# Performance work log

Measured on AMD Instinct MI355X. Metric: run time of the kernel, lower is better.

## Reference

```python
import jax, jax.numpy as jnp
import numpy as np

S = 4096      # total packed tokens
DIM = 1280    # hidden dim
H = 16        # num heads
HD = DIM // H # head dim = 80


def setup_inputs() -> dict:
    key = jax.random.key(0)
    ks = jax.random.split(key, 5)
    hidden_states = jax.random.normal(ks[0], (S, DIM), jnp.float32)
    # realistic rotary tables: [S, HD] with duplicated half-frequencies
    inv_freq = 1.0 / (10000.0 ** (np.arange(0, HD // 2, dtype=np.float64) / (HD // 2)))
    ang = np.arange(S, dtype=np.float64)[:, None] * inv_freq[None, :]          # [S, HD/2]
    emb = np.concatenate([ang, ang], axis=-1)                                   # [S, HD]
    cos = jnp.asarray(np.cos(emb), jnp.float32)
    sin = jnp.asarray(np.sin(emb), jnp.float32)
    scale = 1.0 / np.sqrt(DIM)
    qkv_w = jax.random.normal(ks[1], (3 * DIM, DIM), jnp.float32) * scale
    qkv_b = jax.random.normal(ks[2], (3 * DIM,), jnp.float32) * 0.02
    proj_w = jax.random.normal(ks[3], (DIM, DIM), jnp.float32) * scale
    proj_b = jax.random.normal(ks[4], (DIM,), jnp.float32) * 0.02
    # ragged segment boundaries: must start at 0 and end at S
    cu_seqlens = jnp.asarray([0, 300, 900, 1500, 2300, 2900, 3500, 4000, 4096], jnp.int32)
    return {
        "hidden_states": hidden_states,
        "cos": cos,
        "sin": sin,
        "qkv_w": qkv_w,
        "qkv_b": qkv_b,
        "proj_w": proj_w,
        "proj_b": proj_b,
        "cu_seqlens": cu_seqlens,
    }


def _rotate_half(x):
    x1, x2 = jnp.split(x, 2, axis=-1)
    return jnp.concatenate([-x2, x1], axis=-1)


def reference(hidden_states, cos, sin, qkv_w, qkv_b, proj_w, proj_b, cu_seqlens):
    seq_len, dim = hidden_states.shape
    hd = dim // H
    qkv = (hidden_states @ qkv_w.T + qkv_b).reshape(seq_len, 3, H, hd)
    q, k, v = qkv[:, 0], qkv[:, 1], qkv[:, 2]                 # each [S, H, hd]
    # RoPE in float32, broadcast cos/sin over heads
    c = cos[:, None, :].astype(jnp.float32)
    s = sin[:, None, :].astype(jnp.float32)
    qf = q.astype(jnp.float32)
    kf = k.astype(jnp.float32)
    q = (qf * c + _rotate_half(qf) * s).astype(q.dtype)
    k = (kf * c + _rotate_half(kf) * s).astype(k.dtype)
    # block-diagonal additive mask: segment id per token
    pos = jnp.arange(seq_len)
    seg = jnp.searchsorted(cu_seqlens[1:], pos, side='right')  # [S]
    neg = jnp.finfo(jnp.float32).min
    bias = jnp.where(seg[:, None] == seg[None, :], 0.0, neg)   # [S, S]
    attn = jnp.einsum('shd,thd->hst', q, k) / np.sqrt(hd) + bias[None]
    w = jax.nn.softmax(attn.astype(jnp.float32), axis=-1).astype(q.dtype)
    out = jnp.einsum('hst,thd->shd', w, v).reshape(seq_len, dim)
    return out @ proj_w.T + proj_b
```

## Files before the change

kernel.cpp:

```cpp
#include <hip/hip_runtime.h>
#include <hip/hip_bf16.h>
#include <stdint.h>

#define SQ 4096
#define DM 1280
#define NH 16
#define HDIM 80
#define N_QKV 3840

typedef __attribute__((ext_vector_type(8))) short short8;
typedef __attribute__((ext_vector_type(4))) float f32x4;

__device__ __forceinline__ unsigned short f2bf(float f) {
  union { float f; unsigned int u; } v; v.f = f;
  unsigned int r = v.u + 0x7FFFu + ((v.u >> 16) & 1u);
  return (unsigned short)(r >> 16);
}
__device__ __forceinline__ float bf2f(unsigned short u) {
  union { unsigned int u; float f; } v; v.u = ((unsigned int)u) << 16;
  return v.f;
}

__global__ __launch_bounds__(256) void cvt_all(const float* __restrict__ hidden,
                                               const float* __restrict__ qkv_w,
                                               const float* __restrict__ proj_w,
                                               unsigned short* __restrict__ oh,
                                               unsigned short* __restrict__ oq,
                                               unsigned short* __restrict__ op) {
  int b = blockIdx.x;
  const float* in;
  unsigned short* out;
  int base;
  if (b < 5120) { in = hidden; out = oh; base = b; }
  else if (b < 9920) { in = qkv_w; out = oq; base = b - 5120; }
  else { in = proj_w; out = op; base = b - 9920; }
  int i = base * 256 + threadIdx.x;
  float4 v = reinterpret_cast<const float4*>(in)[i];
  ushort4 o;
  o.x = f2bf(v.x); o.y = f2bf(v.y); o.z = f2bf(v.z); o.w = f2bf(v.w);
  reinterpret_cast<ushort4*>(out)[i] = o;
}

__device__ __forceinline__ void gload_lds16(const void* g, void* l) {
  __builtin_amdgcn_global_load_lds(
      (const __attribute__((address_space(1))) void*)g,
      (__attribute__((address_space(3))) void*)l, 16, 0, 0);
}

template <int OUT_BF16>
__global__ __launch_bounds__(512, 4) void gemm_bt2(const unsigned short* __restrict__ A,
                                                   const unsigned short* __restrict__ B,
                                                   const float* __restrict__ bias,
                                                   void* __restrict__ C, int M, int N, int K,
                                                   int nbx) {
  __shared__ __align__(16) unsigned short As[3][256 * 32];
  __shared__ __align__(16) unsigned short Bs[3][128 * 32];
  const int tid = threadIdx.x;
  const int wave = tid >> 6, lane = tid & 63;
  const int r15 = lane & 15, kg = lane >> 4;
  const int wr = wave >> 1, wc = wave & 1;

  const int b = blockIdx.x;
  const int c = b & 7, i = b >> 3;
  const int by = (c & 3) * 4 + (i & 3);
  const int bx = (c >> 2) * (nbx >> 1) + (i >> 2);
  const int tm = by * 256, tn = bx * 128;

  f32x4 acc[4][4];
#pragma unroll
  for (int x = 0; x < 4; ++x)
#pragma unroll
    for (int j = 0; j < 4; ++j) acc[x][j] = {0.f, 0.f, 0.f, 0.f};

  const int rowt = tid >> 2, k8t = (tid & 3) << 3;
  const unsigned short* Arow0 = A + (size_t)(tm + rowt) * K + k8t;
  const unsigned short* Arow1 = Arow0 + (size_t)128 * K;
  const unsigned short* Brow = B + (size_t)(tn + rowt) * K + k8t;
  const int ldsA0 = tid * 8, ldsA1 = (512 + tid) * 8, ldsB = tid * 8;

  auto stage = [&](int kt, int buf) {
    gload_lds16(Arow0 + kt, &As[buf][ldsA0]);
    gload_lds16(Arow1 + kt, &As[buf][ldsA1]);
    gload_lds16(Brow + kt, &Bs[buf][ldsB]);
  };

  const int nk = K >> 5;
  stage(0, 0);
  stage(32, 1);

  int buf = 0;
  for (int t = 0; t < nk; ++t) {
    if (t + 2 < nk) {
      stage((t + 2) << 5, (buf + 2) % 3);
      asm volatile("s_waitcnt vmcnt(6)" ::: "memory");
    } else if (t + 1 < nk) {
      asm volatile("s_waitcnt vmcnt(3)" ::: "memory");
    } else {
      asm volatile("s_waitcnt vmcnt(0)" ::: "memory");
    }
    __builtin_amdgcn_sched_barrier(0);
    __builtin_amdgcn_s_barrier();

    short8 af[4], bfr[4];
#pragma unroll
    for (int mi = 0; mi < 4; ++mi)
      af[mi] = *reinterpret_cast<const short8*>(&As[buf][(wr * 64 + mi * 16 + r15) * 32 + kg * 8]);
#pragma unroll
    for (int ni = 0; ni < 4; ++ni)
      bfr[ni] = *reinterpret_cast<const short8*>(&Bs[buf][(wc * 64 + ni * 16 + r15) * 32 + kg * 8]);
    __builtin_amdgcn_s_setprio(1);
#pragma unroll
    for (int mi = 0; mi < 4; ++mi)
#pragma unroll
      for (int ni = 0; ni < 4; ++ni)
        acc[mi][ni] = __builtin_amdgcn_mfma_f32_16x16x32_bf16(af[mi], bfr[ni], acc[mi][ni], 0, 0, 0);
    __builtin_amdgcn_s_setprio(0);

    __builtin_amdgcn_s_barrier();
    __builtin_amdgcn_sched_barrier(0);
    buf = (buf + 1) % 3;
  }

#pragma unroll
  for (int mi = 0; mi < 4; ++mi) {
#pragma unroll
    for (int ni = 0; ni < 4; ++ni) {
      int col = tn + wc * 64 + ni * 16 + r15;
      float bv = bias[col];
#pragma unroll
      for (int r = 0; r < 4; ++r) {
        int row = tm + wr * 64 + mi * 16 + kg * 4 + r;
        float v = acc[mi][ni][r] + bv;
        if (OUT_BF16)
          ((unsigned short*)C)[(size_t)row * N + col] = f2bf(v);
        else
          ((float*)C)[(size_t)row * N + col] = v;
      }
    }
  }
}

__global__ __launch_bounds__(256) void rope_v_kernel(unsigned short* __restrict__ qkv,
                                                     const float* __restrict__ cosb,
                                                     const float* __restrict__ sinb,
                                                     unsigned short* __restrict__ Vt) {
  const float SC = 0.1118033988749895f;
  int h = blockIdx.y, s0 = blockIdx.x * 64;
  __shared__ unsigned short vt[64][80];
  for (int e = threadIdx.x; e < 64 * 40; e += 256) {
    int sl = e / 40, dp = e % 40;
    int s = s0 + sl;
    float c = cosb[s * HDIM + dp];
    float sn = sinb[s * HDIM + dp];
    size_t qb = (size_t)s * N_QKV + h * HDIM;
    float q1 = bf2f(qkv[qb + dp]), q2 = bf2f(qkv[qb + dp + 40]);
    qkv[qb + dp] = f2bf((q1 * c - q2 * sn) * SC);
    qkv[qb + dp + 40] = f2bf((q2 * c + q1 * sn) * SC);
    size_t kb = qb + DM;
    float k1 = bf2f(qkv[kb + dp]), k2 = bf2f(qkv[kb + dp + 40]);
    qkv[kb + dp] = f2bf(k1 * c - k2 * sn);
    qkv[kb + dp + 40] = f2bf(k2 * c + k1 * sn);
    size_t vb = qb + 2 * DM;
    vt[sl][dp] = qkv[vb + dp];
    vt[sl][dp + 40] = qkv[vb + dp + 40];
  }
  __syncthreads();
  for (int e = threadIdx.x; e < HDIM * 64; e += 256) {
    int d = e >> 6, sl = e & 63;
    Vt[((size_t)h * HDIM + d) * SQ + s0 + sl] = vt[sl][d];
  }
}

template <int CTRL>
__device__ __forceinline__ float dpp_f(float x) {
  int xi = __builtin_bit_cast(int, x);
  int r = __builtin_amdgcn_update_dpp(xi, xi, CTRL, 0xf, 0xf, true);
  return __builtin_bit_cast(float, r);
}
__device__ __forceinline__ float rowmax16(float x) {
  x = fmaxf(x, dpp_f<0xB1>(x));
  x = fmaxf(x, dpp_f<0x4E>(x));
  x = fmaxf(x, dpp_f<0x141>(x));
  x = fmaxf(x, dpp_f<0x140>(x));
  return x;
}
__device__ __forceinline__ float rowsum16(float x) {
  x += dpp_f<0xB1>(x);
  x += dpp_f<0x4E>(x);
  x += dpp_f<0x141>(x);
  x += dpp_f<0x140>(x);
  return x;
}

__global__ __launch_bounds__(256, 2) void attn_kernel(const unsigned short* __restrict__ qkv,
                                                      const unsigned short* __restrict__ Vt,
                                                      const int* __restrict__ cu, int nseg,
                                                      unsigned short* __restrict__ attn_out) {
  constexpr int PROW = 68;
  __shared__ __align__(16) unsigned char Kl[2][64 * 256];
  __shared__ __align__(16) unsigned char Vl[2][80 * 128];
  __shared__ __align__(16) unsigned short Pl[4][16 * PROW];
  __shared__ int cus[32];
  __shared__ int keyv[64];
  __shared__ unsigned char tile_of_rank[64];

  const int tid = threadIdx.x;
  const int wave = tid >> 6, lane = tid & 63;
  const int r15 = lane & 15, kg = lane >> 4;
  const int s7 = r15 & 7;
  const short8 z8 = {0, 0, 0, 0, 0, 0, 0, 0};

  const int b = blockIdx.x;
  const int xcd = b & 7, j = b >> 3;
  const int h = xcd * 2 + (j >> 6);

  if (tid <= nseg) cus[tid] = cu[tid];
  __syncthreads();

  auto seg_of = [&](int pos) {
    int s2 = 0;
    for (int i2 = 1; i2 < nseg; ++i2)
      if (pos >= cus[i2]) s2 = i2;
    return s2;
  };

  if (tid < 64) {
    int tb = tid * 64;
    int kb = cus[seg_of(tb)] & ~63;
    int ke = cus[seg_of(tb + 63) + 1];
    keyv[tid] = (ke - kb + 63) >> 6;
  }
  __syncthreads();
  if (tid < 64) {
    int mykey = keyv[tid];
    int rank = 0;
    for (int u = 0; u < 64; ++u) {
      int ku = keyv[u];
      rank += (ku > mykey) || (ku == mykey && u < tid);
    }
    tile_of_rank[rank] = (unsigned char)tid;
  }
  __syncthreads();
  const int qt = tile_of_rank[j & 63];

  const int tbase = qt * 64;
  const int wbase = tbase + wave * 16;
  int rs[4], re[4];
#pragma unroll
  for (int r = 0; r < 4; ++r) {
    int sg = seg_of(wbase + kg * 4 + r);
    rs[r] = cus[sg];
    re[r] = cus[sg + 1];
  }
  const int seg_lo = seg_of(wbase), seg_hi = seg_of(wbase + 15);
  const int w_lo = cus[seg_lo], w_hi = cus[seg_hi + 1];
  const int rs_hi = cus[seg_hi], re_lo = cus[seg_lo + 1];

  const int kb0 = cus[seg_of(tbase)] & ~63;
  const int kend = cus[seg_of(tbase + 63) + 1];
  const int nt = (kend - kb0 + 63) >> 6;

  const unsigned short* qp = qkv + (size_t)(wbase + r15) * N_QKV + h * HDIM;
  short8 qf[3];
#pragma unroll
  for (int ds = 0; ds < 3; ++ds) {
    int d0 = ds * 32 + kg * 8;
    qf[ds] = (d0 < HDIM) ? *reinterpret_cast<const short8*>(qp + d0) : z8;
  }

  float m[4] = {-1e30f, -1e30f, -1e30f, -1e30f};
  float l[4] = {0.f, 0.f, 0.f, 0.f};
  f32x4 acc[5];
#pragma unroll
  for (int dg = 0; dg < 5; ++dg) acc[dg] = {0.f, 0.f, 0.f, 0.f};

  const unsigned short* kbase = qkv + DM + (size_t)h * HDIM;
  const unsigned short* vbase = Vt + (size_t)h * HDIM * SQ;
  unsigned short* pw = &Pl[wave][0];
  const int wub = tid & ~63;

  auto issue_stage = [&](int kb, int buf) {
    unsigned char* kd = &Kl[buf][0];
    unsigned char* vd = &Vl[buf][0];
#pragma unroll
    for (int p = 0; p < 4; ++p) {
      int L = p * 256 + tid;
      int row = L >> 4;
      int c = (L & 15) ^ (row & 7);
      int csrc = (c < 10) ? c : 0;
      gload_lds16(kbase + (size_t)(kb + row) * N_QKV + csrc * 8,
                  kd + (p * 256 + wub) * 16);
    }
#pragma unroll
    for (int p = 0; p < 2; ++p) {
      int L = p * 256 + tid;
      int row = L >> 3;
      int c = (L & 7) ^ (row & 7);
      gload_lds16(vbase + (size_t)row * SQ + kb + c * 8,
                  vd + (p * 256 + wub) * 16);
    }
    {
      int L = 512 + (wub >> 1) + (lane & 31);
      int row = L >> 3;
      int c = (L & 7) ^ (row & 7);
      if (lane < 32)
        gload_lds16(vbase + (size_t)row * SQ + kb + c * 8,
                    vd + (512 + (wub >> 1)) * 16);
    }
  };

  issue_stage(kb0, 0);
  int cur = 0;

  for (int t = 0; t < nt; ++t) {
    const int k0 = kb0 + (t << 6);
    if (t + 1 < nt) {
      issue_stage(k0 + 64, cur ^ 1);
      asm volatile("s_waitcnt vmcnt(7)" ::: "memory");
    } else {
      asm volatile("s_waitcnt vmcnt(0)" ::: "memory");
    }
    __builtin_amdgcn_sched_barrier(0);
    __builtin_amdgcn_s_barrier();

    const bool active = (k0 < w_hi) && (k0 + 64 > w_lo);
    if (active) {
      const unsigned char* Kc = &Kl[cur][0];
      const unsigned char* Vc = &Vl[cur][0];

      f32x4 sa[4];
#pragma unroll
      for (int g = 0; g < 4; ++g) sa[g] = {0.f, 0.f, 0.f, 0.f};
#pragma unroll
      for (int g = 0; g < 4; ++g) {
        const unsigned char* kr = Kc + ((g * 16 + r15) << 8);
#pragma unroll
        for (int ds = 0; ds < 3; ++ds) {
          int d0 = ds * 32 + kg * 8;
          short8 kf = (d0 < HDIM)
              ? *reinterpret_cast<const short8*>(kr + (((ds * 4 + kg) ^ s7) << 4))
              : z8;
          sa[g] = __builtin_amdgcn_mfma_f32_16x16x32_bf16(qf[ds], kf, sa[g], 0, 0, 0);
        }
      }

      short8 vf[5][2];
#pragma unroll
      for (int dg = 0; dg < 5; ++dg)
#pragma unroll
        for (int g2 = 0; g2 < 2; ++g2)
          vf[dg][g2] = *reinterpret_cast<const short8*>(
              Vc + ((dg * 16 + r15) << 7) + (((g2 * 4 + kg) ^ s7) << 4));

      const bool interior = (k0 >= rs_hi) && (k0 + 64 <= re_lo);
      float corr[4];
      bool resc;
      if (interior) {
        float mx4[4];
#pragma unroll
        for (int r = 0; r < 4; ++r)
          mx4[r] = rowmax16(fmaxf(fmaxf(sa[0][r], sa[1][r]), fmaxf(sa[2][r], sa[3][r])));
        int defer = (mx4[0] <= m[0] + 8.f) && (mx4[1] <= m[1] + 8.f) &&
                    (mx4[2] <= m[2] + 8.f) && (mx4[3] <= m[3] + 8.f);
        if (__all(defer)) {
          resc = false;
#pragma unroll
          for (int r = 0; r < 4; ++r) {
            unsigned short* prow = pw + (kg * 4 + r) * PROW;
            float sm = 0.f;
#pragma unroll
            for (int g = 0; g < 4; ++g) {
              float pv = __expf(sa[g][r] - m[r]);
              sm += pv;
              prow[g * 16 + r15] = f2bf(pv);
            }
            l[r] += rowsum16(sm);
          }
        } else {
          resc = true;
#pragma unroll
          for (int r = 0; r < 4; ++r) {
            unsigned short* prow = pw + (kg * 4 + r) * PROW;
            float mn = fmaxf(m[r], mx4[r]);
            corr[r] = __expf(m[r] - mn);
            float sm = 0.f;
#pragma unroll
            for (int g = 0; g < 4; ++g) {
              float pv = __expf(sa[g][r] - mn);
              sm += pv;
              prow[g * 16 + r15] = f2bf(pv);
            }
            l[r] = l[r] * corr[r] + rowsum16(sm);
            m[r] = mn;
          }
        }
      } else {
        resc = true;
#pragma unroll
        for (int r = 0; r < 4; ++r) {
          unsigned short* prow = pw + (kg * 4 + r) * PROW;
          float vv[4];
#pragma unroll
          for (int g = 0; g < 4; ++g) {
            int key = k0 + g * 16 + r15;
            vv[g] = (key >= rs[r] && key < re[r]) ? sa[g][r] : -1e30f;
          }
          float mx = rowmax16(fmaxf(fmaxf(vv[0], vv[1]), fmaxf(vv[2], vv[3])));
          float mn = fmaxf(m[r], mx);
          corr[r] = __expf(m[r] - mn);
          float sm = 0.f;
#pragma unroll
          for (int g = 0; g < 4; ++g) {
            float pv = __expf(vv[g] - mn);
            sm += pv;
            prow[g * 16 + r15] = f2bf(pv);
          }
          l[r] = l[r] * corr[r] + rowsum16(sm);
          m[r] = mn;
        }
      }
      if (resc) {
#pragma unroll
        for (int dg = 0; dg < 5; ++dg) {
          f32x4 t2 = acc[dg];
          t2[0] *= corr[0]; t2[1] *= corr[1]; t2[2] *= corr[2]; t2[3] *= corr[3];
          acc[dg] = t2;
        }
      }

      asm volatile("s_waitcnt lgkmcnt(0)" ::: "memory");
      __builtin_amdgcn_sched_barrier(0);
      const unsigned short* prd = pw + r15 * PROW;
      union { short8 v; uint2 d[2]; } pu[2];
#pragma unroll
      for (int g2 = 0; g2 < 2; ++g2) {
        pu[g2].d[0] = *reinterpret_cast<const uint2*>(prd + g2 * 32 + kg * 8);
        pu[g2].d[1] = *reinterpret_cast<const uint2*>(prd + g2 * 32 + kg * 8 + 4);
      }

      __builtin_amdgcn_s_setprio(1);
#pragma unroll
      for (int dg = 0; dg < 5; ++dg)
#pragma unroll
        for (int g2 = 0; g2 < 2; ++g2)
          acc[dg] = __builtin_amdgcn_mfma_f32_16x16x32_bf16(pu[g2].v, vf[dg][g2], acc[dg], 0, 0, 0);
      __builtin_amdgcn_s_setprio(0);
    }

    __builtin_amdgcn_s_barrier();
    cur ^= 1;
  }

#pragma unroll
  for (int r = 0; r < 4; ++r) {
    int row = wbase + kg * 4 + r;
    float inv = 1.0f / l[r];
#pragma unroll
    for (int dg = 0; dg < 5; ++dg)
      attn_out[(size_t)row * DM + h * HDIM + dg * 16 + r15] = f2bf(acc[dg][r] * inv);
  }
}

extern "C" void kernel_launch(void* const* d_in, const int* in_sizes, int n_in,
                              void* d_out, int out_size, void* d_ws, size_t ws_size,
                              hipStream_t stream) {
  const float* hidden = (const float*)d_in[0];
  const float* cosb = (const float*)d_in[1];
  const float* sinb = (const float*)d_in[2];
  const float* qkv_w = (const float*)d_in[3];
  const float* qkv_b = (const float*)d_in[4];
  const float* proj_w = (const float*)d_in[5];
  const float* proj_b = (const float*)d_in[6];
  const int* cu = (const int*)d_in[7];
  int nseg = in_sizes[7] - 1;
  float* out = (float*)d_out;

  char* ws = (char*)d_ws;
  unsigned short* Ah = (unsigned short*)(ws);
  unsigned short* Wq = (unsigned short*)(ws + 10485760);
  unsigned short* Wp = (unsigned short*)(ws + 10485760 + 9830400);
  unsigned short* qkvB = (unsigned short*)(ws + 23592960);
  unsigned short* Vt = (unsigned short*)(ws + 23592960 + 31457280);
  unsigned short* attn_out = Ah;

  cvt_all<<<dim3(11520), dim3(256), 0, stream>>>(hidden, qkv_w, proj_w, Ah, Wq, Wp);
  gemm_bt2<1><<<dim3(480), dim3(512), 0, stream>>>(Ah, Wq, qkv_b, qkvB, SQ, N_QKV, DM, 30);
  rope_v_kernel<<<dim3(64, NH), dim3(256), 0, stream>>>(qkvB, cosb, sinb, Vt);
  attn_kernel<<<dim3(1024), dim3(256), 0, stream>>>(qkvB, Vt, cu, nseg, attn_out);
  gemm_bt2<0><<<dim3(160), dim3(512), 0, stream>>>(attn_out, Wp, proj_b, out, SQ, DM, DM, 10);
}
```

Before: 174.1 us.

## Shrink attention LDS footprint to allow three blocks per CU

Cuts each K tile row in LDS from 256 to 192 bytes, using a 12-chunk layout with a 2-bit XOR swizzle, so only three K loads are issued per stage. The P scratch buffer loses its padding and uses an XOR swizzle, so the PV operands can be read with single 16-byte loads instead of pairs of 8-byte loads. Launch bounds rise from 2 to 3 blocks per CU to use the freed LDS for occupancy. In exchange, register pressure may go up and the smaller swizzles may bring back some bank conflicts.

```diff
diff --git a/kernel.cpp b/kernel.cpp
--- a/kernel.cpp
+++ b/kernel.cpp
@@ -192,14 +192,13 @@
   return x;
 }
 
-__global__ __launch_bounds__(256, 2) void attn_kernel(const unsigned short* __restrict__ qkv,
+__global__ __launch_bounds__(256, 3) void attn_kernel(const unsigned short* __restrict__ qkv,
                                                       const unsigned short* __restrict__ Vt,
                                                       const int* __restrict__ cu, int nseg,
                                                       unsigned short* __restrict__ attn_out) {
-  constexpr int PROW = 68;
-  __shared__ __align__(16) unsigned char Kl[2][64 * 256];
+  __shared__ __align__(16) unsigned char Kl[2][64 * 192];
   __shared__ __align__(16) unsigned char Vl[2][80 * 128];
-  __shared__ __align__(16) unsigned short Pl[4][16 * PROW];
+  __shared__ __align__(16) unsigned short Pl[4][16 * 64];
   __shared__ int cus[32];
   __shared__ int keyv[64];
   __shared__ unsigned char tile_of_rank[64];
@@ -208,6 +207,7 @@
   const int wave = tid >> 6, lane = tid & 63;
   const int r15 = lane & 15, kg = lane >> 4;
   const int s7 = r15 & 7;
+  const int s3 = r15 & 3;
   const short8 z8 = {0, 0, 0, 0, 0, 0, 0, 0};
 
   const int b = blockIdx.x;
@@ -279,18 +279,23 @@
   unsigned short* pw = &Pl[wave][0];
   const int wub = tid & ~63;
 
+  int krow[3], kcs[3];
+#pragma unroll
+  for (int p = 0; p < 3; ++p) {
+    int P = p * 256 + tid;
+    int row = P / 12, pc = P - row * 12;
+    int c = pc ^ (row & 3);
+    krow[p] = row;
+    kcs[p] = (c < 10) ? c : 0;
+  }
+
   auto issue_stage = [&](int kb, int buf) {
     unsigned char* kd = &Kl[buf][0];
     unsigned char* vd = &Vl[buf][0];
 #pragma unroll
-    for (int p = 0; p < 4; ++p) {
-      int L = p * 256 + tid;
-      int row = L >> 4;
-      int c = (L & 15) ^ (row & 7);
-      int csrc = (c < 10) ? c : 0;
-      gload_lds16(kbase + (size_t)(kb + row) * N_QKV + csrc * 8,
+    for (int p = 0; p < 3; ++p)
+      gload_lds16(kbase + (size_t)(kb + krow[p]) * N_QKV + kcs[p] * 8,
                   kd + (p * 256 + wub) * 16);
-    }
 #pragma unroll
     for (int p = 0; p < 2; ++p) {
       int L = p * 256 + tid;
@@ -316,7 +321,7 @@
     const int k0 = kb0 + (t << 6);
     if (t + 1 < nt) {
       issue_stage(k0 + 64, cur ^ 1);
-      asm volatile("s_waitcnt vmcnt(7)" ::: "memory");
+      asm volatile("s_waitcnt vmcnt(6)" ::: "memory");
     } else {
       asm volatile("s_waitcnt vmcnt(0)" ::: "memory");
     }
@@ -333,12 +338,12 @@
       for (int g = 0; g < 4; ++g) sa[g] = {0.f, 0.f, 0.f, 0.f};
 #pragma unroll
       for (int g = 0; g < 4; ++g) {
-        const unsigned char* kr = Kc + ((g * 16 + r15) << 8);
+        const unsigned char* kr = Kc + (g * 16 + r15) * 192;
 #pragma unroll
         for (int ds = 0; ds < 3; ++ds) {
           int d0 = ds * 32 + kg * 8;
           short8 kf = (d0 < HDIM)
-              ? *reinterpret_cast<const short8*>(kr + (((ds * 4 + kg) ^ s7) << 4))
+              ? *reinterpret_cast<const short8*>(kr + (((ds * 4 + kg) ^ s3) << 4))
               : z8;
           sa[g] = __builtin_amdgcn_mfma_f32_16x16x32_bf16(qf[ds], kf, sa[g], 0, 0, 0);
         }
@@ -366,13 +371,14 @@
           resc = false;
 #pragma unroll
           for (int r = 0; r < 4; ++r) {
-            unsigned short* prow = pw + (kg * 4 + r) * PROW;
+            int row = kg * 4 + r, rsw = row & 7;
+            unsigned short* prow = pw + row * 64;
             float sm = 0.f;
 #pragma unroll
             for (int g = 0; g < 4; ++g) {
               float pv = __expf(sa[g][r] - m[r]);
               sm += pv;
-              prow[g * 16 + r15] = f2bf(pv);
+              prow[(((g * 2 + (r15 >> 3)) ^ rsw) << 3) + (r15 & 7)] = f2bf(pv);
             }
             l[r] += rowsum16(sm);
           }
@@ -380,7 +386,8 @@
           resc = true;
 #pragma unroll
           for (int r = 0; r < 4; ++r) {
-            unsigned short* prow = pw + (kg * 4 + r) * PROW;
+            int row = kg * 4 + r, rsw = row & 7;
+            unsigned short* prow = pw + row * 64;
             float mn = fmaxf(m[r], mx4[r]);
             corr[r] = __expf(m[r] - mn);
             float sm = 0.f;
@@ -388,7 +395,7 @@
             for (int g = 0; g < 4; ++g) {
               float pv = __expf(sa[g][r] - mn);
               sm += pv;
-              prow[g * 16 + r15] = f2bf(pv);
+              prow[(((g * 2 + (r15 >> 3)) ^ rsw) << 3) + (r15 & 7)] = f2bf(pv);
             }
             l[r] = l[r] * corr[r] + rowsum16(sm);
             m[r] = mn;
@@ -398,7 +405,8 @@
         resc = true;
 #pragma unroll
         for (int r = 0; r < 4; ++r) {
-          unsigned short* prow = pw + (kg * 4 + r) * PROW;
+          int row = kg * 4 + r, rsw = row & 7;
+          unsigned short* prow = pw + row * 64;
           float vv[4];
 #pragma unroll
           for (int g = 0; g < 4; ++g) {
@@ -413,7 +421,7 @@
           for (int g = 0; g < 4; ++g) {
             float pv = __expf(vv[g] - mn);
             sm += pv;
-            prow[g * 16 + r15] = f2bf(pv);
+            prow[(((g * 2 + (r15 >> 3)) ^ rsw) << 3) + (r15 & 7)] = f2bf(pv);
           }
           l[r] = l[r] * corr[r] + rowsum16(sm);
           m[r] = mn;
@@ -430,20 +438,18 @@
 
       asm volatile("s_waitcnt lgkmcnt(0)" ::: "memory");
       __builtin_amdgcn_sched_barrier(0);
-      const unsigned short* prd = pw + r15 * PROW;
-      union { short8 v; uint2 d[2]; } pu[2];
-#pragma unroll
-      for (int g2 = 0; g2 < 2; ++g2) {
-        pu[g2].d[0] = *reinterpret_cast<const uint2*>(prd + g2 * 32 + kg * 8);
-        pu[g2].d[1] = *reinterpret_cast<const uint2*>(prd + g2 * 32 + kg * 8 + 4);
-      }
+      short8 pu[2];
+#pragma unroll
+      for (int g2 = 0; g2 < 2; ++g2)
+        pu[g2] = *reinterpret_cast<const short8*>(
+            pw + r15 * 64 + (((g2 * 4 + kg) ^ s7) << 3));
 
       __builtin_amdgcn_s_setprio(1);
 #pragma unroll
       for (int dg = 0; dg < 5; ++dg)
 #pragma unroll
         for (int g2 = 0; g2 < 2; ++g2)
-          acc[dg] = __builtin_amdgcn_mfma_f32_16x16x32_bf16(pu[g2].v, vf[dg][g2], acc[dg], 0, 0, 0);
+          acc[dg] = __builtin_amdgcn_mfma_f32_16x16x32_bf16(pu[g2], vf[dg][g2], acc[dg], 0, 0, 0);
       __builtin_amdgcn_s_setprio(0);
     }
 
```

Measured after the change: 268.0 us. +53.9%, slower.
